# Kernel tuning notes

Hardware: AMD Instinct MI355X
Metric: run time of the kernel (lower is better)

Reference implementation:

```python
import jax, jax.numpy as jnp
import numpy as np

D = 1024
H = 16
HD = D // H
FF = 2 * D
EPS = 1e-5


def _ln(x, g, b):
    mu = jnp.mean(x, axis=-1, keepdims=True)
    var = jnp.mean(jnp.square(x - mu), axis=-1, keepdims=True)
    return (x - mu) * jax.lax.rsqrt(var + EPS) * g + b


def setup_inputs() -> dict:
    key = jax.random.key(0)
    ks = jax.random.split(key, 16)
    s = 1.0 / np.sqrt(D)
    sf = 1.0 / np.sqrt(FF)
    inp = {
        "x": jax.random.normal(ks[0], (4, 2048, D), dtype=jnp.float32),
        "Wq": jax.random.uniform(ks[1], (D, D), jnp.float32, -s, s),
        "bq": jnp.zeros((D,), jnp.float32),
        "Wk": jax.random.uniform(ks[2], (D, D), jnp.float32, -s, s),
        "bk": jnp.zeros((D,), jnp.float32),
        "Wv": jax.random.uniform(ks[3], (D, D), jnp.float32, -s, s),
        "bv": jnp.zeros((D,), jnp.float32),
        "Wo": jax.random.uniform(ks[4], (D, D), jnp.float32, -s, s),
        "bo": jnp.zeros((D,), jnp.float32),
        "g1": jnp.ones((D,), jnp.float32),
        "b1": jnp.zeros((D,), jnp.float32),
        "g2": jnp.ones((D,), jnp.float32),
        "b2": jnp.zeros((D,), jnp.float32),
        "W1": jax.random.uniform(ks[5], (D, FF), jnp.float32, -s, s),
        "bf1": jnp.zeros((FF,), jnp.float32),
        "W2": jax.random.uniform(ks[6], (FF, D), jnp.float32, -sf, sf),
        "bf2": jnp.zeros((D,), jnp.float32),
    }
    return inp


def reference(x, Wq, bq, Wk, bk, Wv, bv, Wo, bo, g1, b1, g2, b2, W1, bf1, W2, bf2):
    B, S, _ = x.shape
    scale = HD ** -0.5
    residual = x
    xn = _ln(x, g1, b1)
    # QKV projections -> [B, H, S, HD]
    q = (xn @ Wq + bq).reshape(B, S, H, HD).transpose(0, 2, 1, 3)
    k = (xn @ Wk + bk).reshape(B, S, H, HD).transpose(0, 2, 1, 3)
    v = (xn @ Wv + bv).reshape(B, S, H, HD).transpose(0, 2, 1, 3)
    scores = jnp.einsum("bhqd,bhkd->bhqk", q, k) * scale
    attn = jax.nn.softmax(scores, axis=-1)  # dropout is identity at eval
    ctx = jnp.einsum("bhqk,bhkd->bhqd", attn, v)
    ctx = ctx.transpose(0, 2, 1, 3).reshape(B, S, D)
    x = ctx @ Wo + bo + residual
    residual = x
    xn = _ln(x, g2, b2)
    h = jax.nn.gelu(xn @ W1 + bf1, approximate=False)
    return h @ W2 + bf2 + residual
```

## Files before the change

### kernel.cpp

```cpp
#include <hip/hip_runtime.h>
#include <hip/hip_bf16.h>
#include <math.h>

#define D_MODEL 1024
#define H_NUM 16
#define HD 64
#define FF_DIM 2048
#define SEQ 2048
#define BATCH 4
#define M_TOK 8192

typedef __attribute__((ext_vector_type(8))) short bf16x8;
typedef __attribute__((ext_vector_type(4))) float f32x4;
typedef __attribute__((ext_vector_type(16))) float f32x16;
typedef __attribute__((ext_vector_type(4))) unsigned int uint4v;
typedef __attribute__((ext_vector_type(2))) int int2v;

__device__ __forceinline__ short f2bf(float f) {
  __hip_bfloat16 h = __float2bfloat16(f);
  return *reinterpret_cast<short*>(&h);
}

__device__ __forceinline__ void gload16(const void* g, void* l) {
  __builtin_amdgcn_global_load_lds((const __attribute__((address_space(1))) void*)g,
                                   (__attribute__((address_space(3))) void*)l, 16, 0, 0);
}

__device__ __forceinline__ unsigned cvt_pk_bf16(float lo, float hi) {
  unsigned r;
  asm("v_cvt_pk_bf16_f32 %0, %1, %2" : "=v"(r) : "v"(lo), "v"(hi));
  return r;
}

__device__ __forceinline__ float fexp2(float x) {
  float r;
  asm("v_exp_f32 %0, %1" : "=v"(r) : "v"(x));
  return r;
}

__device__ __forceinline__ float frcp(float x) {
  float r;
  asm("v_rcp_f32 %0, %1" : "=v"(r) : "v"(x));
  return r;
}

#define BARRIER() __builtin_amdgcn_s_barrier()
#define VMC(n)                                   \
  do {                                           \
    asm volatile("s_waitcnt vmcnt(" #n ")");     \
    __builtin_amdgcn_sched_barrier(0);           \
  } while (0)

__global__ __launch_bounds__(256) void prep_fused(
    const float* __restrict__ x, const float* __restrict__ g1,
    const float* __restrict__ b1, short* __restrict__ xn,
    const float* __restrict__ Wq, const float* __restrict__ Wk,
    const float* __restrict__ Wv, const float* __restrict__ Wo,
    const float* __restrict__ W1, const float* __restrict__ W2,
    short* __restrict__ WqkvT, short* __restrict__ WoT,
    short* __restrict__ W1T, short* __restrict__ W2T) {
  __shared__ float tile[64][65];
  if (blockIdx.x < M_TOK) {
    const int row = blockIdx.x;
    const int t = threadIdx.x;
    const float* xr = x + (size_t)row * D_MODEL;
    float4 v = *(const float4*)(xr + t * 4);
    float s = v.x + v.y + v.z + v.w;
    float s2 = v.x * v.x + v.y * v.y + v.z * v.z + v.w * v.w;
#pragma unroll
    for (int m = 1; m < 64; m <<= 1) { s += __shfl_xor(s, m); s2 += __shfl_xor(s2, m); }
    float* ps = &tile[0][0];
    const int wid = t >> 6, lane = t & 63;
    if (lane == 0) { ps[wid] = s; ps[wid + 4] = s2; }
    __syncthreads();
    s = ps[0] + ps[1] + ps[2] + ps[3];
    s2 = ps[4] + ps[5] + ps[6] + ps[7];
    float mu = s * (1.f / D_MODEL);
    float rstd = rsqrtf(s2 * (1.f / D_MODEL) - mu * mu + 1e-5f);
    float4 gv = *(const float4*)(g1 + t * 4);
    float4 bv = *(const float4*)(b1 + t * 4);
    short4 o;
    o.x = f2bf((v.x - mu) * rstd * gv.x + bv.x);
    o.y = f2bf((v.y - mu) * rstd * gv.y + bv.y);
    o.z = f2bf((v.z - mu) * rstd * gv.z + bv.z);
    o.w = f2bf((v.w - mu) * rstd * gv.w + bv.w);
    *(short4*)(xn + (size_t)row * D_MODEL + t * 4) = o;
    return;
  }
  const int bid = blockIdx.x - M_TOK;
  const float* src;
  short* dst;
  int K, N, t;
  if (bid < 256)       { src = Wq; dst = WqkvT;           K = 1024; N = 1024; t = bid; }
  else if (bid < 512)  { src = Wk; dst = WqkvT + 1048576; K = 1024; N = 1024; t = bid - 256; }
  else if (bid < 768)  { src = Wv; dst = WqkvT + 2097152; K = 1024; N = 1024; t = bid - 512; }
  else if (bid < 1024) { src = Wo; dst = WoT;             K = 1024; N = 1024; t = bid - 768; }
  else if (bid < 1536) { src = W1; dst = W1T;             K = 1024; N = 2048; t = bid - 1024; }
  else                 { src = W2; dst = W2T;             K = 2048; N = 1024; t = bid - 1536; }
  const int lg = (N == 2048) ? 5 : 4;
  const int ty = t >> lg, tx = t & ((1 << lg) - 1);
  const int n0 = tx * 64, k0 = ty * 64;
  const int tr = threadIdx.x >> 4;
  const int tc = (threadIdx.x & 15) * 4;
#pragma unroll
  for (int i = 0; i < 4; ++i) {
    int kr = tr + i * 16;
    float4 v = *(const float4*)(src + (size_t)(k0 + kr) * N + n0 + tc);
    tile[kr][tc] = v.x; tile[kr][tc + 1] = v.y; tile[kr][tc + 2] = v.z; tile[kr][tc + 3] = v.w;
  }
  __syncthreads();
#pragma unroll
  for (int i = 0; i < 4; ++i) {
    int r = tr + i * 16;
    short4 o;
    o.x = f2bf(tile[tc][r]);
    o.y = f2bf(tile[tc + 1][r]);
    o.z = f2bf(tile[tc + 2][r]);
    o.w = f2bf(tile[tc + 3][r]);
    *(short4*)(dst + (size_t)(n0 + r) * K + k0 + tc) = o;
  }
}

__global__ __launch_bounds__(256) void transpose_v(const short* __restrict__ src,
                                                   short* __restrict__ dst) {
  __shared__ short t[64][72];
  const int s0 = blockIdx.x * 64;
  const size_t b = (size_t)blockIdx.y * SEQ * HD;
  const int r = threadIdx.x >> 2;
  const int c = (threadIdx.x & 3) * 16;
  *(bf16x8*)&t[r][c] = *(const bf16x8*)(src + b + (size_t)(s0 + r) * HD + c);
  *(bf16x8*)&t[r][c + 8] = *(const bf16x8*)(src + b + (size_t)(s0 + r) * HD + c + 8);
  __syncthreads();
  const int d = threadIdx.x >> 2;
  const int cc = (threadIdx.x & 3) * 16;
  bf16x8 o0, o1;
#pragma unroll
  for (int i = 0; i < 8; ++i) o0[i] = t[cc + i][d];
#pragma unroll
  for (int i = 0; i < 8; ++i) o1[i] = t[cc + 8 + i][d];
  *(bf16x8*)(dst + b + (size_t)d * SEQ + s0 + cc) = o0;
  *(bf16x8*)(dst + b + (size_t)d * SEQ + s0 + cc + 8) = o1;
}

__global__ __launch_bounds__(256) void ln_bf16(const float* __restrict__ x,
                                               const float* __restrict__ g,
                                               const float* __restrict__ b,
                                               short* __restrict__ out) {
  const int row = blockIdx.x;
  const int t = threadIdx.x;
  const float* xr = x + (size_t)row * D_MODEL;
  float4 v = *(const float4*)(xr + t * 4);
  float s = v.x + v.y + v.z + v.w;
  float s2 = v.x * v.x + v.y * v.y + v.z * v.z + v.w * v.w;
#pragma unroll
  for (int m = 1; m < 64; m <<= 1) { s += __shfl_xor(s, m); s2 += __shfl_xor(s2, m); }
  __shared__ float ps[8];
  const int wid = t >> 6, lane = t & 63;
  if (lane == 0) { ps[wid] = s; ps[wid + 4] = s2; }
  __syncthreads();
  s = ps[0] + ps[1] + ps[2] + ps[3];
  s2 = ps[4] + ps[5] + ps[6] + ps[7];
  float mu = s * (1.f / D_MODEL);
  float rstd = rsqrtf(s2 * (1.f / D_MODEL) - mu * mu + 1e-5f);
  float4 gv = *(const float4*)(g + t * 4);
  float4 bv = *(const float4*)(b + t * 4);
  short4 o;
  o.x = f2bf((v.x - mu) * rstd * gv.x + bv.x);
  o.y = f2bf((v.y - mu) * rstd * gv.y + bv.y);
  o.z = f2bf((v.z - mu) * rstd * gv.z + bv.z);
  o.w = f2bf((v.w - mu) * rstd * gv.w + bv.w);
  *(short4*)(out + (size_t)row * D_MODEL + t * 4) = o;
}

template <int FM, int MODE>
__device__ __forceinline__ void gemm_epilogue(f32x4 (&acc)[FM][4], int row0, int col0,
                                              int wr, int wc, int l15, int l4, int BMd2,
                                              const float* bias0, const float* bias1,
                                              const float* bias2, const float* resid,
                                              float* outf, short* outb0, short* outb1,
                                              short* outb2, int N) {
#pragma unroll
  for (int mf = 0; mf < FM; ++mf) {
#pragma unroll
    for (int nf = 0; nf < 4; ++nf) {
      const int rowb = row0 + wr * BMd2 + mf * 16 + (l4 << 2);
      const int col = col0 + wc * 64 + nf * 16 + l15;
      if (MODE == 0) {
        const int which = col >> 10, nn = col & 1023;
        const int hh = nn >> 6, dd = nn & 63;
        const float bias = (which == 0 ? bias0[nn] : which == 1 ? bias1[nn] : bias2[nn]);
        short* o = (which == 0 ? outb0 : which == 1 ? outb1 : outb2);
#pragma unroll
        for (int r = 0; r < 4; ++r) {
          const int row = rowb + r;
          float val = acc[mf][nf][r] + bias;
          if (which == 0) val *= 0.18033688011112042f;
          const int bb = row >> 11, s = row & 2047;
          const size_t dst = (((size_t)((bb << 4) + hh) << 11) + s) * HD + dd;
          o[dst] = f2bf(val);
        }
      } else {
#pragma unroll
        for (int r = 0; r < 4; ++r) {
          const int row = rowb + r;
          float val = acc[mf][nf][r];
          if (MODE == 2) {
            val += bias0[col];
            float a = val * val;
            float c1 = fmaf(a, 0.044715f, 1.0f);
            float arg = (val * 2.302116f) * c1;
            arg = fminf(fmaxf(arg, -60.f), 60.f);
            float e = fexp2(arg);
            float gl = val - val * frcp(e + 1.0f);
            outb0[(size_t)row * N + col] = f2bf(gl);
          } else {
            val += bias0[col] + resid[(size_t)row * N + col];
            outf[(size_t)row * N + col] = val;
          }
        }
      }
    }
  }
}

__device__ __forceinline__ void xcd_map(int id, int nby, int nbx, int& by, int& bx) {
  const int xcd = id & 7, l = id >> 3;
  const int rpx = nby >> 3;
  by = xcd * rpx + (l % rpx);
  bx = l / rpx;
}

template <int BM, int MODE>
__global__ __launch_bounds__(512, 2) void gemm_ring(const short* __restrict__ A,
                                                    const short* __restrict__ Bt,
                                                    const float* __restrict__ bias0,
                                                    const float* __restrict__ bias1,
                                                    const float* __restrict__ bias2,
                                                    const float* resid, float* outf,
                                                    short* outb0, short* outb1, short* outb2,
                                                    int M, int N, int K) {
  constexpr int FM = BM / 32;
  constexpr int GA = BM / 128;
  constexpr int ASLOT = BM * 32;
  constexpr int BSLOT = 256 * 32;
  constexpr int SLOT = ASLOT + BSLOT;
  __shared__ short lds[4 * SLOT];

  const int tid = threadIdx.x;
  const int lane = tid & 63;
  const int wid = tid >> 6;
  const int wr = wid >> 2, wc = wid & 3;
  const int l15 = lane & 15, l4 = lane >> 4;

  int by, bx;
  xcd_map(blockIdx.x, M / BM, N >> 8, by, bx);
  const int row0 = by * BM, col0 = bx * 256;

  f32x4 acc[FM][4];
#pragma unroll
  for (int i = 0; i < FM; ++i)
#pragma unroll
    for (int j = 0; j < 4; ++j) acc[i][j] = (f32x4){0.f, 0.f, 0.f, 0.f};

  const int NH = K >> 5;

  auto STAGE = [&](int h) {
    const int k0 = h * 32;
    short* ab = lds + (h & 3) * SLOT;
#pragma unroll
    for (int s = 0; s < GA; ++s) {
      const int r = s * 128 + (tid >> 2);
      const int g = (tid & 3) ^ ((r >> 1) & 3);
      gload16(A + (size_t)(row0 + r) * K + k0 + g * 8, ab + s * 4096 + tid * 8);
    }
    short* bb = ab + ASLOT;
#pragma unroll
    for (int s = 0; s < 2; ++s) {
      const int r = s * 128 + (tid >> 2);
      const int g = (tid & 3) ^ ((r >> 1) & 3);
      gload16(Bt + (size_t)(col0 + r) * K + k0 + g * 8, bb + s * 4096 + tid * 8);
    }
  };

  bf16x8 Af[FM], Bf[4];

  STAGE(0);
  STAGE(1);
  STAGE(2);

  for (int h = 0; h < NH; ++h) {
    if (h + 2 < NH) {
      if constexpr (GA == 1) { VMC(6); } else { VMC(8); }
    } else if (h + 1 < NH) {
      if constexpr (GA == 1) { VMC(3); } else { VMC(4); }
    } else {
      VMC(0);
    }
    BARRIER();
    if (h + 3 < NH) STAGE(h + 3);
    {
      const short* ab = lds + (h & 3) * SLOT;
#pragma unroll
      for (int i = 0; i < FM; ++i) {
        const int R = wr * (BM / 2) + i * 16 + l15;
        Af[i] = *(const bf16x8*)(ab + (R >> 1) * 64 + (R & 1) * 32 +
                                 ((l4 ^ ((R >> 1) & 3)) << 3));
      }
      const short* bb = ab + ASLOT;
#pragma unroll
      for (int nf = 0; nf < 4; ++nf) {
        const int R = wc * 64 + nf * 16 + l15;
        Bf[nf] = *(const bf16x8*)(bb + (R >> 1) * 64 + (R & 1) * 32 +
                                  ((l4 ^ ((R >> 1) & 3)) << 3));
      }
    }
    __builtin_amdgcn_s_setprio(1);
#pragma unroll
    for (int i = 0; i < FM; ++i)
#pragma unroll
      for (int nf = 0; nf < 4; ++nf)
        acc[i][nf] = __builtin_amdgcn_mfma_f32_16x16x32_bf16(Af[i], Bf[nf], acc[i][nf], 0, 0, 0);
    __builtin_amdgcn_s_setprio(0);
  }

  gemm_epilogue<FM, MODE>(acc, row0, col0, wr, wc, l15, l4, BM / 2,
                          bias0, bias1, bias2, resid, outf, outb0, outb1, outb2, N);
}

template <int MODE>
__global__ __launch_bounds__(512, 4) void gemm_ring2(const short* __restrict__ A,
                                                     const short* __restrict__ Bt,
                                                     const float* __restrict__ bias0,
                                                     const float* __restrict__ bias1,
                                                     const float* __restrict__ bias2,
                                                     const float* resid, float* outf,
                                                     short* outb0, short* outb1, short* outb2,
                                                     int M, int N, int K) {
  constexpr int BM = 128;
  constexpr int FM = 4;
  constexpr int ASLOT = BM * 32;
  constexpr int BSLOT = 256 * 32;
  constexpr int SLOT = ASLOT + BSLOT;
  __shared__ short lds[2 * SLOT];

  const int tid = threadIdx.x;
  const int lane = tid & 63;
  const int wid = tid >> 6;
  const int wr = wid >> 2, wc = wid & 3;
  const int l15 = lane & 15, l4 = lane >> 4;

  int by, bx;
  xcd_map(blockIdx.x, M / BM, N >> 8, by, bx);
  const int row0 = by * BM, col0 = bx * 256;

  f32x4 acc[FM][4];
#pragma unroll
  for (int i = 0; i < FM; ++i)
#pragma unroll
    for (int j = 0; j < 4; ++j) acc[i][j] = (f32x4){0.f, 0.f, 0.f, 0.f};

  const int NH = K >> 5;

  auto STAGE = [&](int h) {
    const int k0 = h * 32;
    short* ab = lds + (h & 1) * SLOT;
    {
      const int r = tid >> 2;
      const int g = (tid & 3) ^ ((r >> 1) & 3);
      gload16(A + (size_t)(row0 + r) * K + k0 + g * 8, ab + tid * 8);
    }
    short* bb = ab + ASLOT;
#pragma unroll
    for (int s = 0; s < 2; ++s) {
      const int r = s * 128 + (tid >> 2);
      const int g = (tid & 3) ^ ((r >> 1) & 3);
      gload16(Bt + (size_t)(col0 + r) * K + k0 + g * 8, bb + s * 4096 + tid * 8);
    }
  };

  bf16x8 Af[FM], Bf[4];

  STAGE(0);
  STAGE(1);

  for (int h = 0; h < NH; ++h) {
    if (h + 1 < NH) { VMC(3); } else { VMC(0); }
    BARRIER();
    {
      const short* ab = lds + (h & 1) * SLOT;
#pragma unroll
      for (int i = 0; i < FM; ++i) {
        const int R = wr * (BM / 2) + i * 16 + l15;
        Af[i] = *(const bf16x8*)(ab + (R >> 1) * 64 + (R & 1) * 32 +
                                 ((l4 ^ ((R >> 1) & 3)) << 3));
      }
      const short* bb = ab + ASLOT;
#pragma unroll
      for (int nf = 0; nf < 4; ++nf) {
        const int R = wc * 64 + nf * 16 + l15;
        Bf[nf] = *(const bf16x8*)(bb + (R >> 1) * 64 + (R & 1) * 32 +
                                  ((l4 ^ ((R >> 1) & 3)) << 3));
      }
    }
    __builtin_amdgcn_s_setprio(1);
#pragma unroll
    for (int i = 0; i < FM; ++i)
#pragma unroll
      for (int nf = 0; nf < 4; ++nf)
        acc[i][nf] = __builtin_amdgcn_mfma_f32_16x16x32_bf16(Af[i], Bf[nf], acc[i][nf], 0, 0, 0);
    __builtin_amdgcn_s_setprio(0);
    BARRIER();
    if (h + 2 < NH) STAGE(h + 2);
  }

  gemm_epilogue<FM, MODE>(acc, row0, col0, wr, wc, l15, l4, BM / 2,
                          bias0, bias1, bias2, resid, outf, outb0, outb1, outb2, N);
}

__global__ __launch_bounds__(512) void attn_swp8(const short* __restrict__ q,
                                                 const short* __restrict__ k,
                                                 const short* __restrict__ vT,
                                                 short* __restrict__ ctx) {
  __shared__ short Ks[2][4096];
  __shared__ short VTs[2][4096];
  const int tid = threadIdx.x;
  const int lane = tid & 63;
  const int wid = tid >> 6;
  const int hi = lane >> 5, l31 = lane & 31, l7 = lane & 7;
  const int bh = blockIdx.x, qt = blockIdx.y;
  const size_t base = (size_t)bh * SEQ * HD;
  const int q0 = qt * 256 + wid * 32;

  bf16x8 qf[4];
#pragma unroll
  for (int ks = 0; ks < 4; ++ks)
    qf[ks] = *(const bf16x8*)(q + base + (size_t)(q0 + l31) * HD + ks * 16 + hi * 8);

  bf16x8 onesv;
#pragma unroll
  for (int i = 0; i < 8; ++i) onesv[i] = (short)0x3F80;

  f32x16 o0, o1, o2;
#pragma unroll
  for (int r = 0; r < 16; ++r) { o0[r] = 0.f; o1[r] = 0.f; o2[r] = 0.f; }

  const int sch = (tid & 7) ^ ((tid >> 3) & 7);

#define STAGE_AT(bi, kt)                                                            \
  {                                                                                 \
    gload16(k + base + (size_t)(kt) * 64 * HD + (size_t)(tid >> 3) * HD + sch * 8,  \
            Ks[bi] + tid * 8);                                                      \
    gload16(vT + base + (size_t)(kt) * 64 + (size_t)(tid >> 3) * SEQ + sch * 8,     \
            VTs[bi] + tid * 8);                                                     \
  }

  STAGE_AT(0, 0);
  STAGE_AT(1, 1);

  for (int kt = 0; kt < SEQ / 64; ++kt) {
    if (kt + 1 < SEQ / 64) { VMC(2); } else { VMC(0); }
    BARRIER();

    const short* Kb = Ks[kt & 1];
    const short* Vb = VTs[kt & 1];

    f32x16 s0, s1;
#pragma unroll
    for (int r = 0; r < 16; ++r) { s0[r] = 0.f; s1[r] = 0.f; }
#pragma unroll
    for (int ks = 0; ks < 4; ++ks) {
      const int ch = ((ks * 2 + hi) ^ l7) << 3;
      bf16x8 ka0 = *(const bf16x8*)(Kb + l31 * 64 + ch);
      bf16x8 ka1 = *(const bf16x8*)(Kb + (32 + l31) * 64 + ch);
      s0 = __builtin_amdgcn_mfma_f32_32x32x16_bf16(ka0, qf[ks], s0, 0, 0, 0);
      s1 = __builtin_amdgcn_mfma_f32_32x32x16_bf16(ka1, qf[ks], s1, 0, 0, 0);
    }

#pragma unroll
    for (int r = 0; r < 16; ++r) s0[r] = fexp2(s0[r]);
#pragma unroll
    for (int r = 0; r < 16; ++r) s1[r] = fexp2(s1[r]);

    uint4v pw[4];
#pragma unroll
    for (int t = 0; t < 2; ++t) {
#pragma unroll
      for (int ks = 0; ks < 2; ++ks) {
        const f32x16& st = t ? s1 : s0;
        unsigned x0 = cvt_pk_bf16(st[8 * ks + 0], st[8 * ks + 1]);
        unsigned x1 = cvt_pk_bf16(st[8 * ks + 2], st[8 * ks + 3]);
        unsigned y0 = cvt_pk_bf16(st[8 * ks + 4], st[8 * ks + 5]);
        unsigned y1 = cvt_pk_bf16(st[8 * ks + 6], st[8 * ks + 7]);
        int2v a0 = __builtin_amdgcn_permlane32_swap((int)y0, (int)x0, false, false);
        int2v a1 = __builtin_amdgcn_permlane32_swap((int)y1, (int)x1, false, false);
        pw[t * 2 + ks] = (uint4v){(unsigned)a0[1], (unsigned)a1[1],
                                  (unsigned)a0[0], (unsigned)a1[0]};
      }
    }

#pragma unroll
    for (int s = 0; s < 4; ++s) {
      bf16x8 pf = __builtin_bit_cast(bf16x8, pw[s]);
      const int ch = ((s * 2 + hi) ^ l7) << 3;
      bf16x8 v0 = *(const bf16x8*)(Vb + l31 * 64 + ch);
      bf16x8 v1 = *(const bf16x8*)(Vb + (32 + l31) * 64 + ch);
      o0 = __builtin_amdgcn_mfma_f32_32x32x16_bf16(v0, pf, o0, 0, 0, 0);
      o1 = __builtin_amdgcn_mfma_f32_32x32x16_bf16(v1, pf, o1, 0, 0, 0);
      o2 = __builtin_amdgcn_mfma_f32_32x32x16_bf16(onesv, pf, o2, 0, 0, 0);
    }

    BARRIER();
    if (kt + 2 < SEQ / 64) STAGE_AT(kt & 1, kt + 2);
  }
#undef STAGE_AT

  const int b = bh >> 4, hh = bh & 15;
  const float inv = 1.f / o2[0];
  const size_t tokoff = ((size_t)(b * SEQ + q0 + l31)) * D_MODEL + hh * HD;
#pragma unroll
  for (int r = 0; r < 16; ++r) {
    const int d = (r & 3) + 8 * (r >> 2) + 4 * hi;
    ctx[tokoff + d] = f2bf(o0[r] * inv);
    ctx[tokoff + 32 + d] = f2bf(o1[r] * inv);
  }
}

extern "C" void kernel_launch(void* const* d_in, const int* in_sizes, int n_in,
                              void* d_out, int out_size, void* d_ws, size_t ws_size,
                              hipStream_t stream) {
  const float* x  = (const float*)d_in[0];
  const float* Wq = (const float*)d_in[1];
  const float* bq = (const float*)d_in[2];
  const float* Wk = (const float*)d_in[3];
  const float* bk = (const float*)d_in[4];
  const float* Wv = (const float*)d_in[5];
  const float* bv = (const float*)d_in[6];
  const float* Wo = (const float*)d_in[7];
  const float* bo = (const float*)d_in[8];
  const float* g1 = (const float*)d_in[9];
  const float* b1 = (const float*)d_in[10];
  const float* g2 = (const float*)d_in[11];
  const float* b2 = (const float*)d_in[12];
  const float* W1 = (const float*)d_in[13];
  const float* bf1 = (const float*)d_in[14];
  const float* W2 = (const float*)d_in[15];
  const float* bf2 = (const float*)d_in[16];

  char* w = (char*)d_ws;
  short* WqkvT = (short*)w; w += (size_t)3072 * 1024 * 2;
  short* WoT   = (short*)w; w += (size_t)1024 * 1024 * 2;
  short* W1T   = (short*)w; w += (size_t)2048 * 1024 * 2;
  short* W2T   = (short*)w; w += (size_t)1024 * 2048 * 2;
  short* xn    = (short*)w; w += (size_t)M_TOK * 1024 * 2;
  short* qb    = (short*)w; w += (size_t)M_TOK * 1024 * 2;
  short* kb    = (short*)w; w += (size_t)M_TOK * 1024 * 2;
  short* vTb   = (short*)w; w += (size_t)M_TOK * 1024 * 2;
  short* ctxb  = (short*)w; w += (size_t)M_TOK * 1024 * 2;
  short* xn2   = (short*)w; w += (size_t)M_TOK * 1024 * 2;
  short* hb    = (short*)w; w += (size_t)M_TOK * 2048 * 2;
  short* vb    = hb;

  dim3 blk(256);

  prep_fused<<<dim3(M_TOK + 2048), blk, 0, stream>>>(
      x, g1, b1, xn, Wq, Wk, Wv, Wo, W1, W2, WqkvT, WoT, W1T, W2T);

  gemm_ring2<0><<<dim3(12 * 64), dim3(512), 0, stream>>>(
      xn, WqkvT, bq, bk, bv, nullptr, nullptr, qb, kb, vb, M_TOK, 3072, 1024);

  transpose_v<<<dim3(SEQ / 64, BATCH * H_NUM), blk, 0, stream>>>(vb, vTb);

  attn_swp8<<<dim3(64, SEQ / 256), dim3(512), 0, stream>>>(qb, kb, vTb, ctxb);

  gemm_ring<128, 1><<<dim3(4 * 64), dim3(512), 0, stream>>>(
      ctxb, WoT, bo, nullptr, nullptr, x, (float*)d_out, nullptr, nullptr, nullptr,
      M_TOK, 1024, 1024);

  ln_bf16<<<M_TOK, blk, 0, stream>>>((const float*)d_out, g2, b2, xn2);

  gemm_ring<256, 2><<<dim3(8 * 32), dim3(512), 0, stream>>>(
      xn2, W1T, bf1, nullptr, nullptr, nullptr, nullptr, hb, nullptr, nullptr,
      M_TOK, 2048, 1024);

  gemm_ring<128, 3><<<dim3(4 * 64), dim3(512), 0, stream>>>(
      hb, W2T, bf2, nullptr, nullptr, (const float*)d_out, (float*)d_out,
      nullptr, nullptr, nullptr, M_TOK, 1024, 2048);
}
```

Baseline: 287.6 us.

## Unify GEMMs on double-buffered ring2 with BN template, compute softmax denom by row-sum

Removes the 4-stage gemm_ring kernel and routes the output projection, FFN1 and FFN2 GEMMs through gemm_ring2, which is now templated on the N-tile width (128 or 256). The N=1024 GEMMs get 128x128 tiles and twice as many blocks, and FFN1 moves from 256-row to 128-row tiles. This trades deeper pipelining for higher occupancy and better wave counts. Separately, the attention kernel drops the extra MFMA against a ones vector used for the softmax denominator and instead accumulates row sums in registers with a permlane32 swap.

```diff
diff --git a/kernel.cpp b/kernel.cpp
--- a/kernel.cpp
+++ b/kernel.cpp
@@ -172,8 +172,8 @@
   *(short4*)(out + (size_t)row * D_MODEL + t * 4) = o;
 }
 
-template <int FM, int MODE>
-__device__ __forceinline__ void gemm_epilogue(f32x4 (&acc)[FM][4], int row0, int col0,
+template <int FM, int NB, int MODE>
+__device__ __forceinline__ void gemm_epilogue(f32x4 (&acc)[FM][NB], int row0, int col0,
                                               int wr, int wc, int l15, int l4, int BMd2,
                                               const float* bias0, const float* bias1,
                                               const float* bias2, const float* resid,
@@ -182,9 +182,9 @@
 #pragma unroll
   for (int mf = 0; mf < FM; ++mf) {
 #pragma unroll
-    for (int nf = 0; nf < 4; ++nf) {
+    for (int nf = 0; nf < NB; ++nf) {
       const int rowb = row0 + wr * BMd2 + mf * 16 + (l4 << 2);
-      const int col = col0 + wc * 64 + nf * 16 + l15;
+      const int col = col0 + wc * (NB * 16) + nf * 16 + l15;
       if (MODE == 0) {
         const int which = col >> 10, nn = col & 1023;
         const int hh = nn >> 6, dd = nn & 63;
@@ -230,104 +230,7 @@
   bx = l / rpx;
 }
 
-template <int BM, int MODE>
-__global__ __launch_bounds__(512, 2) void gemm_ring(const short* __restrict__ A,
-                                                    const short* __restrict__ Bt,
-                                                    const float* __restrict__ bias0,
-                                                    const float* __restrict__ bias1,
-                                                    const float* __restrict__ bias2,
-                                                    const float* resid, float* outf,
-                                                    short* outb0, short* outb1, short* outb2,
-                                                    int M, int N, int K) {
-  constexpr int FM = BM / 32;
-  constexpr int GA = BM / 128;
-  constexpr int ASLOT = BM * 32;
-  constexpr int BSLOT = 256 * 32;
-  constexpr int SLOT = ASLOT + BSLOT;
-  __shared__ short lds[4 * SLOT];
-
-  const int tid = threadIdx.x;
-  const int lane = tid & 63;
-  const int wid = tid >> 6;
-  const int wr = wid >> 2, wc = wid & 3;
-  const int l15 = lane & 15, l4 = lane >> 4;
-
-  int by, bx;
-  xcd_map(blockIdx.x, M / BM, N >> 8, by, bx);
-  const int row0 = by * BM, col0 = bx * 256;
-
-  f32x4 acc[FM][4];
-#pragma unroll
-  for (int i = 0; i < FM; ++i)
-#pragma unroll
-    for (int j = 0; j < 4; ++j) acc[i][j] = (f32x4){0.f, 0.f, 0.f, 0.f};
-
-  const int NH = K >> 5;
-
-  auto STAGE = [&](int h) {
-    const int k0 = h * 32;
-    short* ab = lds + (h & 3) * SLOT;
-#pragma unroll
-    for (int s = 0; s < GA; ++s) {
-      const int r = s * 128 + (tid >> 2);
-      const int g = (tid & 3) ^ ((r >> 1) & 3);
-      gload16(A + (size_t)(row0 + r) * K + k0 + g * 8, ab + s * 4096 + tid * 8);
-    }
-    short* bb = ab + ASLOT;
-#pragma unroll
-    for (int s = 0; s < 2; ++s) {
-      const int r = s * 128 + (tid >> 2);
-      const int g = (tid & 3) ^ ((r >> 1) & 3);
-      gload16(Bt + (size_t)(col0 + r) * K + k0 + g * 8, bb + s * 4096 + tid * 8);
-    }
-  };
-
-  bf16x8 Af[FM], Bf[4];
-
-  STAGE(0);
-  STAGE(1);
-  STAGE(2);
-
-  for (int h = 0; h < NH; ++h) {
-    if (h + 2 < NH) {
-      if constexpr (GA == 1) { VMC(6); } else { VMC(8); }
-    } else if (h + 1 < NH) {
-      if constexpr (GA == 1) { VMC(3); } else { VMC(4); }
-    } else {
-      VMC(0);
-    }
-    BARRIER();
-    if (h + 3 < NH) STAGE(h + 3);
-    {
-      const short* ab = lds + (h & 3) * SLOT;
-#pragma unroll
-      for (int i = 0; i < FM; ++i) {
-        const int R = wr * (BM / 2) + i * 16 + l15;
-        Af[i] = *(const bf16x8*)(ab + (R >> 1) * 64 + (R & 1) * 32 +
-                                 ((l4 ^ ((R >> 1) & 3)) << 3));
-      }
-      const short* bb = ab + ASLOT;
-#pragma unroll
-      for (int nf = 0; nf < 4; ++nf) {
-        const int R = wc * 64 + nf * 16 + l15;
-        Bf[nf] = *(const bf16x8*)(bb + (R >> 1) * 64 + (R & 1) * 32 +
-                                  ((l4 ^ ((R >> 1) & 3)) << 3));
-      }
-    }
-    __builtin_amdgcn_s_setprio(1);
-#pragma unroll
-    for (int i = 0; i < FM; ++i)
-#pragma unroll
-      for (int nf = 0; nf < 4; ++nf)
-        acc[i][nf] = __builtin_amdgcn_mfma_f32_16x16x32_bf16(Af[i], Bf[nf], acc[i][nf], 0, 0, 0);
-    __builtin_amdgcn_s_setprio(0);
-  }
-
-  gemm_epilogue<FM, MODE>(acc, row0, col0, wr, wc, l15, l4, BM / 2,
-                          bias0, bias1, bias2, resid, outf, outb0, outb1, outb2, N);
-}
-
-template <int MODE>
+template <int BN, int MODE>
 __global__ __launch_bounds__(512, 4) void gemm_ring2(const short* __restrict__ A,
                                                      const short* __restrict__ Bt,
                                                      const float* __restrict__ bias0,
@@ -338,8 +241,9 @@
                                                      int M, int N, int K) {
   constexpr int BM = 128;
   constexpr int FM = 4;
+  constexpr int NB = BN / 64;
   constexpr int ASLOT = BM * 32;
-  constexpr int BSLOT = 256 * 32;
+  constexpr int BSLOT = BN * 32;
   constexpr int SLOT = ASLOT + BSLOT;
   __shared__ short lds[2 * SLOT];
 
@@ -350,14 +254,14 @@
   const int l15 = lane & 15, l4 = lane >> 4;
 
   int by, bx;
-  xcd_map(blockIdx.x, M / BM, N >> 8, by, bx);
-  const int row0 = by * BM, col0 = bx * 256;
-
-  f32x4 acc[FM][4];
+  xcd_map(blockIdx.x, M / BM, N / BN, by, bx);
+  const int row0 = by * BM, col0 = bx * BN;
+
+  f32x4 acc[FM][NB];
 #pragma unroll
   for (int i = 0; i < FM; ++i)
 #pragma unroll
-    for (int j = 0; j < 4; ++j) acc[i][j] = (f32x4){0.f, 0.f, 0.f, 0.f};
+    for (int j = 0; j < NB; ++j) acc[i][j] = (f32x4){0.f, 0.f, 0.f, 0.f};
 
   const int NH = K >> 5;
 
@@ -371,20 +275,24 @@
     }
     short* bb = ab + ASLOT;
 #pragma unroll
-    for (int s = 0; s < 2; ++s) {
+    for (int s = 0; s < BN / 128; ++s) {
       const int r = s * 128 + (tid >> 2);
       const int g = (tid & 3) ^ ((r >> 1) & 3);
       gload16(Bt + (size_t)(col0 + r) * K + k0 + g * 8, bb + s * 4096 + tid * 8);
     }
   };
 
-  bf16x8 Af[FM], Bf[4];
+  bf16x8 Af[FM], Bf[NB];
 
   STAGE(0);
   STAGE(1);
 
   for (int h = 0; h < NH; ++h) {
-    if (h + 1 < NH) { VMC(3); } else { VMC(0); }
+    if (h + 1 < NH) {
+      if constexpr (BN == 256) { VMC(3); } else { VMC(2); }
+    } else {
+      VMC(0);
+    }
     BARRIER();
     {
       const short* ab = lds + (h & 1) * SLOT;
@@ -396,8 +304,8 @@
       }
       const short* bb = ab + ASLOT;
 #pragma unroll
-      for (int nf = 0; nf < 4; ++nf) {
-        const int R = wc * 64 + nf * 16 + l15;
+      for (int nf = 0; nf < NB; ++nf) {
+        const int R = wc * (NB * 16) + nf * 16 + l15;
         Bf[nf] = *(const bf16x8*)(bb + (R >> 1) * 64 + (R & 1) * 32 +
                                   ((l4 ^ ((R >> 1) & 3)) << 3));
       }
@@ -406,15 +314,15 @@
 #pragma unroll
     for (int i = 0; i < FM; ++i)
 #pragma unroll
-      for (int nf = 0; nf < 4; ++nf)
+      for (int nf = 0; nf < NB; ++nf)
         acc[i][nf] = __builtin_amdgcn_mfma_f32_16x16x32_bf16(Af[i], Bf[nf], acc[i][nf], 0, 0, 0);
     __builtin_amdgcn_s_setprio(0);
     BARRIER();
     if (h + 2 < NH) STAGE(h + 2);
   }
 
-  gemm_epilogue<FM, MODE>(acc, row0, col0, wr, wc, l15, l4, BM / 2,
-                          bias0, bias1, bias2, resid, outf, outb0, outb1, outb2, N);
+  gemm_epilogue<FM, NB, MODE>(acc, row0, col0, wr, wc, l15, l4, BM / 2,
+                              bias0, bias1, bias2, resid, outf, outb0, outb1, outb2, N);
 }
 
 __global__ __launch_bounds__(512) void attn_swp8(const short* __restrict__ q,
@@ -436,13 +344,10 @@
   for (int ks = 0; ks < 4; ++ks)
     qf[ks] = *(const bf16x8*)(q + base + (size_t)(q0 + l31) * HD + ks * 16 + hi * 8);
 
-  bf16x8 onesv;
-#pragma unroll
-  for (int i = 0; i < 8; ++i) onesv[i] = (short)0x3F80;
-
-  f32x16 o0, o1, o2;
-#pragma unroll
-  for (int r = 0; r < 16; ++r) { o0[r] = 0.f; o1[r] = 0.f; o2[r] = 0.f; }
+  f32x16 o0, o1;
+#pragma unroll
+  for (int r = 0; r < 16; ++r) { o0[r] = 0.f; o1[r] = 0.f; }
+  float lreg = 0.f;
 
   const int sch = (tid & 7) ^ ((tid >> 3) & 7);
 
@@ -480,6 +385,17 @@
     for (int r = 0; r < 16; ++r) s0[r] = fexp2(s0[r]);
 #pragma unroll
     for (int r = 0; r < 16; ++r) s1[r] = fexp2(s1[r]);
+
+    {
+      float rs = 0.f;
+#pragma unroll
+      for (int r = 0; r < 16; ++r) rs += s0[r];
+#pragma unroll
+      for (int r = 0; r < 16; ++r) rs += s1[r];
+      int2v ss = __builtin_amdgcn_permlane32_swap(__builtin_bit_cast(int, rs),
+                                                  __builtin_bit_cast(int, rs), false, false);
+      lreg += __builtin_bit_cast(float, ss[0]) + __builtin_bit_cast(float, ss[1]);
+    }
 
     uint4v pw[4];
 #pragma unroll
@@ -506,7 +422,6 @@
       bf16x8 v1 = *(const bf16x8*)(Vb + (32 + l31) * 64 + ch);
       o0 = __builtin_amdgcn_mfma_f32_32x32x16_bf16(v0, pf, o0, 0, 0, 0);
       o1 = __builtin_amdgcn_mfma_f32_32x32x16_bf16(v1, pf, o1, 0, 0, 0);
-      o2 = __builtin_amdgcn_mfma_f32_32x32x16_bf16(onesv, pf, o2, 0, 0, 0);
     }
 
     BARRIER();
@@ -515,7 +430,7 @@
 #undef STAGE_AT
 
   const int b = bh >> 4, hh = bh & 15;
-  const float inv = 1.f / o2[0];
+  const float inv = 1.f / lreg;
   const size_t tokoff = ((size_t)(b * SEQ + q0 + l31)) * D_MODEL + hh * HD;
 #pragma unroll
   for (int r = 0; r < 16; ++r) {
@@ -565,24 +480,24 @@
   prep_fused<<<dim3(M_TOK + 2048), blk, 0, stream>>>(
       x, g1, b1, xn, Wq, Wk, Wv, Wo, W1, W2, WqkvT, WoT, W1T, W2T);
 
-  gemm_ring2<0><<<dim3(12 * 64), dim3(512), 0, stream>>>(
+  gemm_ring2<256, 0><<<dim3(12 * 64), dim3(512), 0, stream>>>(
       xn, WqkvT, bq, bk, bv, nullptr, nullptr, qb, kb, vb, M_TOK, 3072, 1024);
 
   transpose_v<<<dim3(SEQ / 64, BATCH * H_NUM), blk, 0, stream>>>(vb, vTb);
 
   attn_swp8<<<dim3(64, SEQ / 256), dim3(512), 0, stream>>>(qb, kb, vTb, ctxb);
 
-  gemm_ring<128, 1><<<dim3(4 * 64), dim3(512), 0, stream>>>(
+  gemm_ring2<128, 1><<<dim3(8 * 64), dim3(512), 0, stream>>>(
       ctxb, WoT, bo, nullptr, nullptr, x, (float*)d_out, nullptr, nullptr, nullptr,
       M_TOK, 1024, 1024);
 
   ln_bf16<<<M_TOK, blk, 0, stream>>>((const float*)d_out, g2, b2, xn2);
 
-  gemm_ring<256, 2><<<dim3(8 * 32), dim3(512), 0, stream>>>(
+  gemm_ring2<256, 2><<<dim3(8 * 64), dim3(512), 0, stream>>>(
       xn2, W1T, bf1, nullptr, nullptr, nullptr, nullptr, hb, nullptr, nullptr,
       M_TOK, 2048, 1024);
 
-  gemm_ring<128, 3><<<dim3(4 * 64), dim3(512), 0, stream>>>(
+  gemm_ring2<128, 3><<<dim3(8 * 64), dim3(512), 0, stream>>>(
       hb, W2T, bf2, nullptr, nullptr, (const float*)d_out, (float*)d_out,
       nullptr, nullptr, nullptr, M_TOK, 1024, 2048);
 }
```

Measured after the change: 290.6 us. No clear change (+1.0%).
